# Kernel optimization log

Measured on AMD Instinct MI355X. Metric: run time of the kernel, lower is better.

## Reference

```python
import jax, jax.numpy as jnp
import numpy as np

E = 1024
H = 16
F = 4096
B, S = 4, 2048
LN_EPS = 1e-5


def setup_inputs() -> dict:
    key = jax.random.key(0)
    ks = jax.random.split(key, 12)
    sE = 1.0 / np.sqrt(E)
    sF = 1.0 / np.sqrt(F)
    return {
        "x": jax.random.normal(ks[0], (B, S, E), dtype=jnp.float32),
        # attention projections (torch Linear weight layout [out,in], bias=False)
        "Wq": jax.random.uniform(ks[1], (E, E), jnp.float32, -sE, sE),
        "Wk": jax.random.uniform(ks[2], (E, E), jnp.float32, -sE, sE),
        "Wv": jax.random.uniform(ks[3], (E, E), jnp.float32, -sE, sE),
        "Wo": jax.random.uniform(ks[4], (E, E), jnp.float32, -sE, sE),
        # LayerNorms
        "g1": jnp.ones((E,), jnp.float32),
        "b1": jnp.zeros((E,), jnp.float32),
        "g2": jnp.ones((E,), jnp.float32),
        "b2": jnp.zeros((E,), jnp.float32),
        # FFN (classical): linear1 [F,E], linear2 [E,F]
        "W1": jax.random.uniform(ks[5], (F, E), jnp.float32, -sE, sE),
        "bb1": jax.random.uniform(ks[6], (F,), jnp.float32, -sE, sE),
        "W2": jax.random.uniform(ks[7], (E, F), jnp.float32, -sF, sF),
        "bb2": jax.random.uniform(ks[8], (F,), jnp.float32, -sF, sF)[:E] * 0 + jax.random.uniform(ks[9], (E,), jnp.float32, -sF, sF),
    }


def _layernorm(x, g, b):
    mu = jnp.mean(x, axis=-1, keepdims=True)
    var = jnp.mean(jnp.square(x - mu), axis=-1, keepdims=True)
    return (x - mu) * jax.lax.rsqrt(var + LN_EPS) * g + b


def reference(x, Wq, Wk, Wv, Wo, g1, b1, g2, b2, W1, bb1, W2, bb2):
    b, s, _ = x.shape
    hd = E // H
    # projections: torch Linear is x @ W.T
    q = (x @ Wq.T).reshape(b, s, H, hd).transpose(0, 2, 1, 3)  # [B,H,S,hd]
    k = (x @ Wk.T).reshape(b, s, H, hd).transpose(0, 2, 1, 3)
    v = (x @ Wv.T).reshape(b, s, H, hd).transpose(0, 2, 1, 3)
    scores = jnp.einsum('bhqd,bhkd->bhqk', q, k) / jnp.sqrt(jnp.float32(hd))
    probs = jax.nn.softmax(scores, axis=-1)
    attn = jnp.einsum('bhqk,bhkd->bhqd', probs, v)
    attn = attn.transpose(0, 2, 1, 3).reshape(b, s, E)
    attn_out = attn @ Wo.T
    # residual + LN (dropout=0 / eval)
    h = _layernorm(x + attn_out, g1, b1)
    # FFN
    ffn = jax.nn.relu(h @ W1.T + bb1) @ W2.T + bb2
    return _layernorm(h + ffn, g2, b2)
```

## Files before the change

### kernel.cpp

```cpp
#include <hip/hip_runtime.h>
#include <stdint.h>

#define E_DIM   1024
#define H_NUM   16
#define HD      64
#define F_DIM   4096
#define B_NUM   4
#define S_LEN   2048
#define M_ROWS  (B_NUM * S_LEN)
#define QKV_LD  3072

typedef unsigned short u16;
typedef __bf16 bf16_t;
typedef bf16_t  bf16x8 __attribute__((ext_vector_type(8)));
typedef u16     u16x8  __attribute__((ext_vector_type(8)));
typedef float   f32x4  __attribute__((ext_vector_type(4)));
typedef float   f32x16 __attribute__((ext_vector_type(16)));
typedef unsigned u32x4 __attribute__((ext_vector_type(4)));

#define AS1 __attribute__((address_space(1)))
#define AS3 __attribute__((address_space(3)))

__device__ __forceinline__ void gload_lds16(const void* g, void* l) {
    __builtin_amdgcn_global_load_lds((AS1 void*)g, (AS3 void*)l, 16, 0, 0);
}

__device__ __forceinline__ u16 f2b(float f) {
    union { float f; unsigned u; } a; a.f = f;
    unsigned u = a.u + 0x7fffu + ((a.u >> 16) & 1u);
    return (u16)(u >> 16);
}
__device__ __forceinline__ float b2f(u16 v) {
    union { unsigned u; float f; } a; a.u = ((unsigned)v) << 16;
    return a.f;
}

__device__ __forceinline__ unsigned cvt_pk_bf16(float lo, float hi) {
    unsigned r;
    asm("v_cvt_pk_bf16_f32 %0, %1, %2" : "=v"(r) : "v"(lo), "v"(hi));
    return r;
}

__device__ __forceinline__ int swz_c(int row) {
    return ((row & 7) << 4) ^ ((row & 8) << 2);
}
__device__ __forceinline__ int swz8(int row) {
    return (row & 7) << 4;
}

#define VM_WAIT(n) asm volatile("s_waitcnt vmcnt(" #n ")" ::: "memory")

struct CastArgs {
    const float* src[7];
    u16* dst[7];
    unsigned cum4[8];
};

__global__ __launch_bounds__(256) void cast_multi(CastArgs a) {
    const int total = a.cum4[7];
    const int stride = gridDim.x * blockDim.x;
    for (int i = blockIdx.x * blockDim.x + threadIdx.x; i < total; i += stride) {
        int s = 0;
#pragma unroll
        for (int k = 1; k < 7; ++k) s += (i >= (int)a.cum4[k]);
        const int off = i - (int)a.cum4[s];
        float4 v = reinterpret_cast<const float4*>(a.src[s])[off];
        ushort4 o;
        o.x = f2b(v.x); o.y = f2b(v.y); o.z = f2b(v.z); o.w = f2b(v.w);
        reinterpret_cast<ushort4*>(a.dst[s])[off] = o;
    }
}

__device__ __forceinline__ void store_c(float* C, size_t idx, float v) { C[idx] = v; }
__device__ __forceinline__ void store_c(u16* C, size_t idx, float v)   { C[idx] = f2b(v); }

template <typename OutT, bool RELU, bool HASBIAS, int K>
__global__ __launch_bounds__(512, 4)
void gemm2(const u16* __restrict__ A, const u16* __restrict__ B,
           OutT* __restrict__ C, const float* __restrict__ bias,
           int M, int N) {
    constexpr int NT = K / 32;
    __shared__ __align__(16) char smem[3 * 24576];

    const int tid  = threadIdx.x;
    const int lane = tid & 63, wave = tid >> 6;
    const int lr   = lane & 15, kh = lane >> 4;
    const int wr   = wave >> 2, wc = wave & 3;

    const int nwg = gridDim.x * gridDim.y;
    int wg = blockIdx.y * gridDim.x + blockIdx.x;
    const int cpx = nwg >> 3;
    wg = (wg & 7) * cpx + (wg >> 3);
    const int bx = wg % gridDim.x, by = wg / gridDim.x;
    const int row0 = by * 128, col0 = bx * 256;

    const int srow = tid >> 2, scolb = (tid & 3) * 16;
    const char* Ag  = (const char*)(A + (size_t)(row0 + srow) * K) + scolb;
    const char* Bg0 = (const char*)(B + (size_t)(col0 + srow) * K) + scolb;
    const char* Bg1 = (const char*)(B + (size_t)(col0 + 128 + srow) * K) + scolb;
    const int ldsw = wave * 1024;

    auto stage = [&](int t) {
        char* s = smem + (t % 3) * 24576;
        const size_t ko = (size_t)t * 64;
        gload_lds16(Ag + ko,  s + ldsw);
        gload_lds16(Bg0 + ko, s + 8192 + ldsw);
        gload_lds16(Bg1 + ko, s + 16384 + ldsw);
    };

    f32x4 acc[4][4] = {};
    stage(0); stage(1);

    for (int t = 0; t < NT; ++t) {
        if (t + 1 < NT) VM_WAIT(3);
        else            VM_WAIT(0);
        __builtin_amdgcn_s_barrier();
        __builtin_amdgcn_sched_barrier(0);
        if (t + 2 < NT) stage(t + 2);

        const char* s = smem + (t % 3) * 24576;
        bf16x8 af[4], bf[4];
#pragma unroll
        for (int m = 0; m < 4; ++m)
            af[m] = *(const bf16x8*)(s + (wr * 64 + m * 16 + lr) * 64 + kh * 16);
#pragma unroll
        for (int n = 0; n < 4; ++n)
            bf[n] = *(const bf16x8*)(s + 8192 + (wc * 64 + n * 16 + lr) * 64 + kh * 16);

        __builtin_amdgcn_s_setprio(1);
#pragma unroll
        for (int m = 0; m < 4; ++m)
#pragma unroll
            for (int n = 0; n < 4; ++n)
                acc[m][n] = __builtin_amdgcn_mfma_f32_16x16x32_bf16(af[m], bf[n], acc[m][n], 0, 0, 0);
        __builtin_amdgcn_s_setprio(0);
    }

#pragma unroll
    for (int m = 0; m < 4; ++m) {
#pragma unroll
        for (int n = 0; n < 4; ++n) {
            int col = col0 + wc * 64 + n * 16 + lr;
            float bv = 0.f;
            if constexpr (HASBIAS) bv = bias[col];
#pragma unroll
            for (int r = 0; r < 4; ++r) {
                int row = row0 + wr * 64 + m * 16 + kh * 4 + r;
                float v = acc[m][n][r] + bv;
                if constexpr (RELU) v = fmaxf(v, 0.f);
                store_c(C, (size_t)row * N + col, v);
            }
        }
    }
}

template <typename OutT, bool RELU, bool HASBIAS, int K>
__global__ __launch_bounds__(256, 3)
void gemm2h(const u16* __restrict__ A, const u16* __restrict__ B,
            OutT* __restrict__ C, const float* __restrict__ bias,
            int M, int N) {
    constexpr int NT = K / 32;
    __shared__ __align__(16) char smem[3 * 16384];

    const int tid  = threadIdx.x;
    const int lane = tid & 63, wave = tid >> 6;
    const int lr   = lane & 15, kh = lane >> 4;
    const int wr   = wave >> 1, wc = wave & 1;

    const int nwg = gridDim.x * gridDim.y;
    int wg = blockIdx.y * gridDim.x + blockIdx.x;
    const int cpx = nwg >> 3;
    wg = (wg & 7) * cpx + (wg >> 3);
    const int bx = wg % gridDim.x, by = wg / gridDim.x;
    const int row0 = by * 128, col0 = bx * 128;

    const int srow = tid >> 2;
    const int scolb = (tid & 3) * 16;
    const char* Ag = (const char*)(A + (size_t)(row0 + srow) * K) + scolb;
    const char* Bg = (const char*)(B + (size_t)(col0 + srow) * K) + scolb;
    const size_t rstep = (size_t)64 * K * 2;

    auto do_stage = [&](int t) {
        char* s = smem + (t % 3) * 16384;
        const size_t ko = (size_t)t * 64;
        gload_lds16(Ag + ko,         s + tid * 16);
        gload_lds16(Ag + rstep + ko, s + 4096 + tid * 16);
        gload_lds16(Bg + ko,         s + 8192 + tid * 16);
        gload_lds16(Bg + rstep + ko, s + 12288 + tid * 16);
    };

    f32x4 acc[4][4] = {};
    do_stage(0); do_stage(1);

    for (int t = 0; t < NT; ++t) {
        if (t + 1 < NT) VM_WAIT(4);
        else            VM_WAIT(0);
        __builtin_amdgcn_s_barrier();
        __builtin_amdgcn_sched_barrier(0);
        if (t + 2 < NT) do_stage(t + 2);

        const char* s = smem + (t % 3) * 16384;
        bf16x8 af[4], bf[4];
#pragma unroll
        for (int m = 0; m < 4; ++m)
            af[m] = *(const bf16x8*)(s + (wr * 64 + m * 16 + lr) * 64 + kh * 16);
#pragma unroll
        for (int n = 0; n < 4; ++n)
            bf[n] = *(const bf16x8*)(s + 8192 + (wc * 64 + n * 16 + lr) * 64 + kh * 16);

        __builtin_amdgcn_s_setprio(1);
#pragma unroll
        for (int m = 0; m < 4; ++m)
#pragma unroll
            for (int n = 0; n < 4; ++n)
                acc[m][n] = __builtin_amdgcn_mfma_f32_16x16x32_bf16(af[m], bf[n], acc[m][n], 0, 0, 0);
        __builtin_amdgcn_s_setprio(0);
    }

#pragma unroll
    for (int m = 0; m < 4; ++m) {
#pragma unroll
        for (int n = 0; n < 4; ++n) {
            int col = col0 + wc * 64 + n * 16 + lr;
            float bv = 0.f;
            if constexpr (HASBIAS) bv = bias[col];
#pragma unroll
            for (int r = 0; r < 4; ++r) {
                int row = row0 + wr * 64 + m * 16 + kh * 4 + r;
                float v = acc[m][n][r] + bv;
                if constexpr (RELU) v = fmaxf(v, 0.f);
                store_c(C, (size_t)row * N + col, v);
            }
        }
    }
}

#define SC_LOG2E 0.1803368801111204f

__global__ __launch_bounds__(256, 4)
void attn_kernel(const u16* __restrict__ QKV, u16* __restrict__ Ob) {
    __shared__ char Ks[2][64 * 128];
    __shared__ char Vt[2][64 * 128];

    const int tid  = threadIdx.x;
    const int lane = tid & 63, wave = tid >> 6;
    const int l31  = lane & 31, hi = lane >> 5;
    const int q0   = blockIdx.x * 128;
    const int h    = blockIdx.y;
    const int b    = blockIdx.z;

    const u16* Q  = QKV;
    const u16* Kp = QKV + 1024;
    const u16* V  = QKV + 2048;

    const size_t qrow = (size_t)(b * S_LEN + q0 + wave * 32 + l31);
    bf16x8 qf[4];
#pragma unroll
    for (int c = 0; c < 4; ++c) {
        qf[c] = *(const bf16x8*)(Q + qrow * QKV_LD + h * HD + c * 16 + hi * 8);
#pragma unroll
        for (int j = 0; j < 8; ++j)
            qf[c][j] = (bf16_t)((float)qf[c][j] * SC_LOG2E);
    }

    f32x16 o0 = {}, o1 = {};
    float l_run = 0.f;

    const u16* Vg = V + (size_t)(b * S_LEN) * QKV_LD + h * HD;
    const char* Kg = (const char*)(Kp + (size_t)(b * S_LEN) * QKV_LD + h * HD);

    int kst_row[2], kst_colb[2], kst_lds[2];
#pragma unroll
    for (int j = 0; j < 2; ++j) {
        const int ob = (wave * 2 + j) * 1024 + lane * 16;
        kst_row[j]  = ob >> 7;
        kst_colb[j] = (ob & 127) ^ swz_c(kst_row[j]);
        kst_lds[j]  = (wave * 2 + j) * 1024;
    }
    const int vkv = wave * 16;
    const int krd = l31 * 128;
    const int vrd = l31 * 128;

    u16 vst[16];
#pragma unroll
    for (int j = 0; j < 2; ++j)
        gload_lds16(Kg + (size_t)kst_row[j] * (QKV_LD * 2) + kst_colb[j], Ks[0] + kst_lds[j]);
    {
        const u16* vp = Vg + (size_t)vkv * QKV_LD + lane;
#pragma unroll
        for (int i = 0; i < 16; ++i) vst[i] = vp[(size_t)i * QKV_LD];
        u16x8 va, vb;
#pragma unroll
        for (int i = 0; i < 4; ++i) {
            va[i] = vst[i];     va[4 + i] = vst[8 + i];
            vb[i] = vst[4 + i]; vb[4 + i] = vst[12 + i];
        }
        *(u16x8*)(Vt[0] + lane * 128 + ((vkv * 2) ^ swz8(lane)))      = va;
        *(u16x8*)(Vt[0] + lane * 128 + ((vkv * 2 + 16) ^ swz8(lane))) = vb;
    }
    __syncthreads();

    const int NT = S_LEN / 64;
    for (int t = 0; t < NT; ++t) {
        const int cur = t & 1;
        if (t < NT - 1) {
            const int kv0n = (t + 1) * 64;
#pragma unroll
            for (int j = 0; j < 2; ++j)
                gload_lds16(Kg + (size_t)(kv0n + kst_row[j]) * (QKV_LD * 2) + kst_colb[j],
                            Ks[cur ^ 1] + kst_lds[j]);
            const u16* vp = Vg + (size_t)(kv0n + vkv) * QKV_LD + lane;
#pragma unroll
            for (int i = 0; i < 16; ++i) vst[i] = vp[(size_t)i * QKV_LD];
        }

#pragma unroll
        for (int half = 0; half < 2; ++half) {
            const char* ksb = Ks[cur] + half * 4096 + krd;
            f32x16 st = {};
#pragma unroll
            for (int c = 0; c < 4; ++c) {
                bf16x8 kf = *(const bf16x8*)(ksb + ((c * 32 + hi * 16) ^ swz_c(l31)));
                st = __builtin_amdgcn_mfma_f32_32x32x16_bf16(kf, qf[c], st, 0, 0, 0);
            }

            float rs0 = 0.f, rs1 = 0.f, rs2 = 0.f, rs3 = 0.f;
#pragma unroll
            for (int i = 0; i < 16; i += 4) {
                st[i]     = exp2f(st[i]);
                st[i + 1] = exp2f(st[i + 1]);
                st[i + 2] = exp2f(st[i + 2]);
                st[i + 3] = exp2f(st[i + 3]);
                rs0 += st[i]; rs1 += st[i + 1]; rs2 += st[i + 2]; rs3 += st[i + 3];
            }
            float rs = (rs0 + rs1) + (rs2 + rs3);
            rs += __shfl_xor(rs, 32);
            l_run += rs;

            unsigned w[8];
#pragma unroll
            for (int i = 0; i < 8; ++i) w[i] = cvt_pk_bf16(st[2 * i], st[2 * i + 1]);

#pragma unroll
            for (int cc = 0; cc < 2; ++cc) {
                u32x4 fw;
                fw[0] = w[4 * cc];     fw[1] = w[4 * cc + 1];
                fw[2] = w[4 * cc + 2]; fw[3] = w[4 * cc + 3];
                bf16x8 pf = __builtin_bit_cast(bf16x8, fw);
                const int colb = (half * 64 + cc * 32 + hi * 16) ^ swz8(l31);
                bf16x8 v0 = *(const bf16x8*)(Vt[cur] + vrd + colb);
                bf16x8 v1 = *(const bf16x8*)(Vt[cur] + 4096 + vrd + colb);
                o0 = __builtin_amdgcn_mfma_f32_32x32x16_bf16(v0, pf, o0, 0, 0, 0);
                o1 = __builtin_amdgcn_mfma_f32_32x32x16_bf16(v1, pf, o1, 0, 0, 0);
            }
        }

        if (t < NT - 1) {
            u16x8 va, vb;
#pragma unroll
            for (int i = 0; i < 4; ++i) {
                va[i] = vst[i];     va[4 + i] = vst[8 + i];
                vb[i] = vst[4 + i]; vb[4 + i] = vst[12 + i];
            }
            *(u16x8*)(Vt[cur ^ 1] + lane * 128 + ((vkv * 2) ^ swz8(lane)))      = va;
            *(u16x8*)(Vt[cur ^ 1] + lane * 128 + ((vkv * 2 + 16) ^ swz8(lane))) = vb;
        }
        __syncthreads();
    }

    const float inv = 1.0f / l_run;
    unsigned m0[16], xx[16];
#pragma unroll
    for (int g = 0; g < 4; ++g)
#pragma unroll
        for (int u = 0; u < 2; ++u) {
            int r = g * 4 + 2 * u;
            m0[2 * g + u]     = cvt_pk_bf16(o0[r] * inv, o0[r + 1] * inv);
            m0[8 + 2 * g + u] = cvt_pk_bf16(o1[r] * inv, o1[r + 1] * inv);
        }
#pragma unroll
    for (int i = 0; i < 16; ++i) xx[i] = __shfl_xor(m0[i], 32);

    {
        unsigned full[8], sec[8];
#pragma unroll
        for (int g = 0; g < 4; ++g) {
            full[2 * g + 0] = hi ? xx[8 + 2 * g]     : m0[2 * g];
            full[2 * g + 1] = hi ? xx[8 + 2 * g + 1] : m0[2 * g + 1];
            sec[2 * g + 0]  = hi ? m0[8 + 2 * g]     : xx[2 * g];
            sec[2 * g + 1]  = hi ? m0[8 + 2 * g + 1] : xx[2 * g + 1];
        }
        u32x4 out0, out1, out2, out3;
        out0[0] = full[0]; out0[1] = full[1]; out0[2] = sec[0]; out0[3] = sec[1];
        out1[0] = full[2]; out1[1] = full[3]; out1[2] = sec[2]; out1[3] = sec[3];
        out2[0] = full[4]; out2[1] = full[5]; out2[2] = sec[4]; out2[3] = sec[5];
        out3[0] = full[6]; out3[1] = full[7]; out3[2] = sec[6]; out3[3] = sec[7];
        u16* op = Ob + qrow * E_DIM + h * HD + hi * 32;
        *(u32x4*)(op)      = out0;
        *(u32x4*)(op + 8)  = out1;
        *(u32x4*)(op + 16) = out2;
        *(u32x4*)(op + 24) = out3;
    }
}

template <typename XA, typename XB>
__device__ __forceinline__ float4 ld4(const XA* p, size_t idx) {
    if constexpr (sizeof(XA) == 2) {
        ushort4 v = reinterpret_cast<const ushort4*>(p)[idx];
        float4 o; o.x = b2f(v.x); o.y = b2f(v.y); o.z = b2f(v.z); o.w = b2f(v.w);
        return o;
    } else {
        return reinterpret_cast<const float4*>(p)[idx];
    }
}

template <typename XA, typename XB>
__global__ __launch_bounds__(256)
void add_ln(const XA* __restrict__ xa, const XB* __restrict__ xb2,
            const float* __restrict__ g, const float* __restrict__ be,
            float* __restrict__ of, u16* __restrict__ ob) {
    const int row = blockIdx.x;
    const int t = threadIdx.x;
    const int lane = t & 63, wave = t >> 6;

    float4 va = ld4<XA, XB>(xa + (size_t)row * E_DIM, t);
    float4 vb = ld4<XB, XA>(xb2 + (size_t)row * E_DIM, t);
    float v0 = va.x + vb.x, v1 = va.y + vb.y, v2 = va.z + vb.z, v3 = va.w + vb.w;
    float s  = v0 + v1 + v2 + v3;
    float s2 = v0 * v0 + v1 * v1 + v2 * v2 + v3 * v3;
#pragma unroll
    for (int m = 32; m >= 1; m >>= 1) {
        s  += __shfl_xor(s, m);
        s2 += __shfl_xor(s2, m);
    }
    __shared__ float red[8];
    if (lane == 0) { red[wave] = s; red[4 + wave] = s2; }
    __syncthreads();
    s  = red[0] + red[1] + red[2] + red[3];
    s2 = red[4] + red[5] + red[6] + red[7];

    float mu   = s * (1.0f / E_DIM);
    float var  = s2 * (1.0f / E_DIM) - mu * mu;
    float rstd = rsqrtf(var + 1e-5f);

    float4 gg = reinterpret_cast<const float4*>(g)[t];
    float4 bb = reinterpret_cast<const float4*>(be)[t];
    float y0 = (v0 - mu) * rstd * gg.x + bb.x;
    float y1 = (v1 - mu) * rstd * gg.y + bb.y;
    float y2 = (v2 - mu) * rstd * gg.z + bb.z;
    float y3 = (v3 - mu) * rstd * gg.w + bb.w;
    if (of) {
        float4 o; o.x = y0; o.y = y1; o.z = y2; o.w = y3;
        reinterpret_cast<float4*>(of + (size_t)row * E_DIM)[t] = o;
    }
    if (ob) {
        ushort4 o;
        o.x = f2b(y0); o.y = f2b(y1); o.z = f2b(y2); o.w = f2b(y3);
        reinterpret_cast<ushort4*>(ob + (size_t)row * E_DIM)[t] = o;
    }
}

extern "C" void kernel_launch(void* const* d_in, const int* in_sizes, int n_in,
                              void* d_out, int out_size, void* d_ws, size_t ws_size,
                              hipStream_t stream) {
    const float* x   = (const float*)d_in[0];
    const float* Wq  = (const float*)d_in[1];
    const float* Wk  = (const float*)d_in[2];
    const float* Wv  = (const float*)d_in[3];
    const float* Wo  = (const float*)d_in[4];
    const float* g1  = (const float*)d_in[5];
    const float* b1  = (const float*)d_in[6];
    const float* g2  = (const float*)d_in[7];
    const float* b2  = (const float*)d_in[8];
    const float* W1  = (const float*)d_in[9];
    const float* bb1 = (const float*)d_in[10];
    const float* W2  = (const float*)d_in[11];
    const float* bb2 = (const float*)d_in[12];
    float* out = (float*)d_out;

    char* ws = (char*)d_ws;
    const size_t MB = 1024ull * 1024ull;
    u16* wqkvb = (u16*)(ws + 0 * MB);
    u16* wob   = (u16*)(ws + 6 * MB);
    u16* w1b   = (u16*)(ws + 8 * MB);
    u16* w2b   = (u16*)(ws + 16 * MB);
    u16* xb    = (u16*)(ws + 24 * MB);
    u16* qkvb  = (u16*)(ws + 40 * MB);
    u16* attnb = (u16*)(ws + 88 * MB);
    u16* attno = (u16*)(ws + 104 * MB);
    u16* hb    = (u16*)(ws + 136 * MB);
    u16* ffn1  = (u16*)(ws + 24 * MB);
    u16* y2b   = (u16*)(ws + 104 * MB);

    dim3 blk(256);

    CastArgs ca;
    ca.src[0] = x;   ca.dst[0] = xb;
    ca.src[1] = Wq;  ca.dst[1] = wqkvb;
    ca.src[2] = Wk;  ca.dst[2] = wqkvb + E_DIM * E_DIM;
    ca.src[3] = Wv;  ca.dst[3] = wqkvb + 2 * E_DIM * E_DIM;
    ca.src[4] = Wo;  ca.dst[4] = wob;
    ca.src[5] = W1;  ca.dst[5] = w1b;
    ca.src[6] = W2;  ca.dst[6] = w2b;
    unsigned n4[7] = {M_ROWS * E_DIM / 4, E_DIM * E_DIM / 4, E_DIM * E_DIM / 4,
                      E_DIM * E_DIM / 4, E_DIM * E_DIM / 4, F_DIM * E_DIM / 4,
                      E_DIM * F_DIM / 4};
    ca.cum4[0] = 0;
    for (int i = 0; i < 7; ++i) ca.cum4[i + 1] = ca.cum4[i] + n4[i];
    cast_multi<<<dim3(2048), blk, 0, stream>>>(ca);

    dim3 blk5(512);
    gemm2<u16, false, false, E_DIM><<<dim3(QKV_LD / 256, M_ROWS / 128), blk5, 0, stream>>>(
        xb, wqkvb, qkvb, nullptr, M_ROWS, QKV_LD);

    attn_kernel<<<dim3(S_LEN / 128, H_NUM, B_NUM), blk, 0, stream>>>(qkvb, attnb);

    gemm2h<u16, false, false, E_DIM><<<dim3(E_DIM / 128, M_ROWS / 128), blk, 0, stream>>>(
        attnb, wob, attno, nullptr, M_ROWS, E_DIM);

    add_ln<float, u16><<<dim3(M_ROWS), blk, 0, stream>>>(x, attno, g1, b1, nullptr, hb);

    gemm2<u16, true, true, E_DIM><<<dim3(F_DIM / 256, M_ROWS / 128), blk5, 0, stream>>>(
        hb, w1b, ffn1, bb1, M_ROWS, F_DIM);

    gemm2h<u16, false, true, F_DIM><<<dim3(E_DIM / 128, M_ROWS / 128), blk, 0, stream>>>(
        ffn1, w2b, y2b, bb2, M_ROWS, E_DIM);

    add_ln<u16, u16><<<dim3(M_ROWS), blk, 0, stream>>>(hb, y2b, g2, b2, out, nullptr);
}
```

Measured before the change: 392.4 us.

## Emit V pre-transposed and swizzled from QKV GEMM; fold softmax scale into Wq

The QKV projection GEMM now writes the V columns directly into a per-head transposed, swizzled global layout. This lets the attention kernel stream V tiles into LDS with async global_load_lds, in place of strided 2-byte gathers followed by register shuffles and LDS stores. The softmax scale times log2(e) is folded into Wq during the bf16 cast, which removes the per-element Q scaling in attention. The cost is a scattered 8-byte-store epilogue for V in the GEMM, an extra workspace buffer, and a slightly different rounding order for the Q scaling.

```diff
diff --git a/kernel.cpp b/kernel.cpp
--- a/kernel.cpp
+++ b/kernel.cpp
@@ -49,10 +49,12 @@
 }
 
 #define VM_WAIT(n) asm volatile("s_waitcnt vmcnt(" #n ")" ::: "memory")
+#define SC_LOG2E 0.1803368801111204f
 
 struct CastArgs {
     const float* src[7];
     u16* dst[7];
+    float scale[7];
     unsigned cum4[8];
 };
 
@@ -64,9 +66,10 @@
 #pragma unroll
         for (int k = 1; k < 7; ++k) s += (i >= (int)a.cum4[k]);
         const int off = i - (int)a.cum4[s];
+        const float sc = a.scale[s];
         float4 v = reinterpret_cast<const float4*>(a.src[s])[off];
         ushort4 o;
-        o.x = f2b(v.x); o.y = f2b(v.y); o.z = f2b(v.z); o.w = f2b(v.w);
+        o.x = f2b(v.x * sc); o.y = f2b(v.y * sc); o.z = f2b(v.z * sc); o.w = f2b(v.w * sc);
         reinterpret_cast<ushort4*>(a.dst[s])[off] = o;
     }
 }
@@ -74,11 +77,11 @@
 __device__ __forceinline__ void store_c(float* C, size_t idx, float v) { C[idx] = v; }
 __device__ __forceinline__ void store_c(u16* C, size_t idx, float v)   { C[idx] = f2b(v); }
 
-template <typename OutT, bool RELU, bool HASBIAS, int K>
+template <typename OutT, bool RELU, bool HASBIAS, int K, bool VSPLIT>
 __global__ __launch_bounds__(512, 4)
 void gemm2(const u16* __restrict__ A, const u16* __restrict__ B,
            OutT* __restrict__ C, const float* __restrict__ bias,
-           int M, int N) {
+           char* __restrict__ VtG, int M, int N) {
     constexpr int NT = K / 32;
     __shared__ __align__(16) char smem[3 * 24576];
 
@@ -134,6 +137,31 @@
             for (int n = 0; n < 4; ++n)
                 acc[m][n] = __builtin_amdgcn_mfma_f32_16x16x32_bf16(af[m], bf[n], acc[m][n], 0, 0, 0);
         __builtin_amdgcn_s_setprio(0);
+    }
+
+    if (VSPLIT && col0 >= 2048) {
+#pragma unroll
+        for (int m = 0; m < 4; ++m) {
+#pragma unroll
+            for (int n = 0; n < 4; ++n) {
+                const int colv = col0 - 2048 + wc * 64 + n * 16 + lr;
+                const int h = colv >> 6, d = colv & 63;
+                const int rowq = row0 + wr * 64 + m * 16 + kh * 4;
+                const int bq = rowq >> 11, sq = rowq & 2047;
+                const int kvt = sq >> 6, kl = sq & 63;
+                const int g = kl >> 4, qb = kl & 12;
+                const int slotq = ((qb & 4) << 1) | ((qb & 8) >> 1) | (qb & 3);
+                const size_t byte_off = ((size_t)((bq * H_NUM + h) * HD + d) << 12)
+                                        + kvt * 128 + ((((g << 4) + slotq) << 1) ^ swz8(d));
+                const u16 p0 = f2b(acc[m][n][0]), p1 = f2b(acc[m][n][1]);
+                const u16 p2 = f2b(acc[m][n][2]), p3 = f2b(acc[m][n][3]);
+                uint2 pk;
+                pk.x = (unsigned)p0 | ((unsigned)p1 << 16);
+                pk.y = (unsigned)p2 | ((unsigned)p3 << 16);
+                *(uint2*)(VtG + byte_off) = pk;
+            }
+        }
+        return;
     }
 
 #pragma unroll
@@ -235,10 +263,9 @@
     }
 }
 
-#define SC_LOG2E 0.1803368801111204f
-
 __global__ __launch_bounds__(256, 4)
-void attn_kernel(const u16* __restrict__ QKV, u16* __restrict__ Ob) {
+void attn_kernel(const u16* __restrict__ QKV, const char* __restrict__ VtG,
+                 u16* __restrict__ Ob) {
     __shared__ char Ks[2][64 * 128];
     __shared__ char Vt[2][64 * 128];
 
@@ -251,52 +278,35 @@
 
     const u16* Q  = QKV;
     const u16* Kp = QKV + 1024;
-    const u16* V  = QKV + 2048;
 
     const size_t qrow = (size_t)(b * S_LEN + q0 + wave * 32 + l31);
     bf16x8 qf[4];
 #pragma unroll
-    for (int c = 0; c < 4; ++c) {
+    for (int c = 0; c < 4; ++c)
         qf[c] = *(const bf16x8*)(Q + qrow * QKV_LD + h * HD + c * 16 + hi * 8);
-#pragma unroll
-        for (int j = 0; j < 8; ++j)
-            qf[c][j] = (bf16_t)((float)qf[c][j] * SC_LOG2E);
-    }
 
     f32x16 o0 = {}, o1 = {};
     float l_run = 0.f;
 
-    const u16* Vg = V + (size_t)(b * S_LEN) * QKV_LD + h * HD;
-    const char* Kg = (const char*)(Kp + (size_t)(b * S_LEN) * QKV_LD + h * HD);
-
-    int kst_row[2], kst_colb[2], kst_lds[2];
+    const char* Kg  = (const char*)(Kp + (size_t)(b * S_LEN) * QKV_LD + h * HD);
+    const char* Vgb = VtG + ((size_t)((b * H_NUM + h) * HD) << 12);
+
+    int st_row[2], st_colb[2], st_lds[2], kst_colb[2];
 #pragma unroll
     for (int j = 0; j < 2; ++j) {
         const int ob = (wave * 2 + j) * 1024 + lane * 16;
-        kst_row[j]  = ob >> 7;
-        kst_colb[j] = (ob & 127) ^ swz_c(kst_row[j]);
-        kst_lds[j]  = (wave * 2 + j) * 1024;
-    }
-    const int vkv = wave * 16;
+        st_row[j]   = ob >> 7;
+        st_colb[j]  = ob & 127;
+        kst_colb[j] = (ob & 127) ^ swz_c(st_row[j]);
+        st_lds[j]   = (wave * 2 + j) * 1024;
+    }
     const int krd = l31 * 128;
     const int vrd = l31 * 128;
 
-    u16 vst[16];
-#pragma unroll
-    for (int j = 0; j < 2; ++j)
-        gload_lds16(Kg + (size_t)kst_row[j] * (QKV_LD * 2) + kst_colb[j], Ks[0] + kst_lds[j]);
-    {
-        const u16* vp = Vg + (size_t)vkv * QKV_LD + lane;
-#pragma unroll
-        for (int i = 0; i < 16; ++i) vst[i] = vp[(size_t)i * QKV_LD];
-        u16x8 va, vb;
-#pragma unroll
-        for (int i = 0; i < 4; ++i) {
-            va[i] = vst[i];     va[4 + i] = vst[8 + i];
-            vb[i] = vst[4 + i]; vb[4 + i] = vst[12 + i];
-        }
-        *(u16x8*)(Vt[0] + lane * 128 + ((vkv * 2) ^ swz8(lane)))      = va;
-        *(u16x8*)(Vt[0] + lane * 128 + ((vkv * 2 + 16) ^ swz8(lane))) = vb;
+#pragma unroll
+    for (int j = 0; j < 2; ++j) {
+        gload_lds16(Kg + (size_t)st_row[j] * (QKV_LD * 2) + kst_colb[j], Ks[0] + st_lds[j]);
+        gload_lds16(Vgb + (size_t)st_row[j] * 4096 + st_colb[j],         Vt[0] + st_lds[j]);
     }
     __syncthreads();
 
@@ -306,12 +316,12 @@
         if (t < NT - 1) {
             const int kv0n = (t + 1) * 64;
 #pragma unroll
-            for (int j = 0; j < 2; ++j)
-                gload_lds16(Kg + (size_t)(kv0n + kst_row[j]) * (QKV_LD * 2) + kst_colb[j],
-                            Ks[cur ^ 1] + kst_lds[j]);
-            const u16* vp = Vg + (size_t)(kv0n + vkv) * QKV_LD + lane;
-#pragma unroll
-            for (int i = 0; i < 16; ++i) vst[i] = vp[(size_t)i * QKV_LD];
+            for (int j = 0; j < 2; ++j) {
+                gload_lds16(Kg + (size_t)(kv0n + st_row[j]) * (QKV_LD * 2) + kst_colb[j],
+                            Ks[cur ^ 1] + st_lds[j]);
+                gload_lds16(Vgb + (size_t)st_row[j] * 4096 + (t + 1) * 128 + st_colb[j],
+                            Vt[cur ^ 1] + st_lds[j]);
+            }
         }
 
 #pragma unroll
@@ -353,17 +363,6 @@
                 o0 = __builtin_amdgcn_mfma_f32_32x32x16_bf16(v0, pf, o0, 0, 0, 0);
                 o1 = __builtin_amdgcn_mfma_f32_32x32x16_bf16(v1, pf, o1, 0, 0, 0);
             }
-        }
-
-        if (t < NT - 1) {
-            u16x8 va, vb;
-#pragma unroll
-            for (int i = 0; i < 4; ++i) {
-                va[i] = vst[i];     va[4 + i] = vst[8 + i];
-                vb[i] = vst[4 + i]; vb[4 + i] = vst[12 + i];
-            }
-            *(u16x8*)(Vt[cur ^ 1] + lane * 128 + ((vkv * 2) ^ swz8(lane)))      = va;
-            *(u16x8*)(Vt[cur ^ 1] + lane * 128 + ((vkv * 2 + 16) ^ swz8(lane))) = vb;
         }
         __syncthreads();
     }
@@ -489,19 +488,20 @@
     u16* attnb = (u16*)(ws + 88 * MB);
     u16* attno = (u16*)(ws + 104 * MB);
     u16* hb    = (u16*)(ws + 136 * MB);
+    char* VtG  = (ws + 152 * MB);
     u16* ffn1  = (u16*)(ws + 24 * MB);
     u16* y2b   = (u16*)(ws + 104 * MB);
 
     dim3 blk(256);
 
     CastArgs ca;
-    ca.src[0] = x;   ca.dst[0] = xb;
-    ca.src[1] = Wq;  ca.dst[1] = wqkvb;
-    ca.src[2] = Wk;  ca.dst[2] = wqkvb + E_DIM * E_DIM;
-    ca.src[3] = Wv;  ca.dst[3] = wqkvb + 2 * E_DIM * E_DIM;
-    ca.src[4] = Wo;  ca.dst[4] = wob;
-    ca.src[5] = W1;  ca.dst[5] = w1b;
-    ca.src[6] = W2;  ca.dst[6] = w2b;
+    ca.src[0] = x;   ca.dst[0] = xb;                            ca.scale[0] = 1.f;
+    ca.src[1] = Wq;  ca.dst[1] = wqkvb;                         ca.scale[1] = SC_LOG2E;
+    ca.src[2] = Wk;  ca.dst[2] = wqkvb + E_DIM * E_DIM;         ca.scale[2] = 1.f;
+    ca.src[3] = Wv;  ca.dst[3] = wqkvb + 2 * E_DIM * E_DIM;     ca.scale[3] = 1.f;
+    ca.src[4] = Wo;  ca.dst[4] = wob;                           ca.scale[4] = 1.f;
+    ca.src[5] = W1;  ca.dst[5] = w1b;                           ca.scale[5] = 1.f;
+    ca.src[6] = W2;  ca.dst[6] = w2b;                           ca.scale[6] = 1.f;
     unsigned n4[7] = {M_ROWS * E_DIM / 4, E_DIM * E_DIM / 4, E_DIM * E_DIM / 4,
                       E_DIM * E_DIM / 4, E_DIM * E_DIM / 4, F_DIM * E_DIM / 4,
                       E_DIM * F_DIM / 4};
@@ -510,18 +510,18 @@
     cast_multi<<<dim3(2048), blk, 0, stream>>>(ca);
 
     dim3 blk5(512);
-    gemm2<u16, false, false, E_DIM><<<dim3(QKV_LD / 256, M_ROWS / 128), blk5, 0, stream>>>(
-        xb, wqkvb, qkvb, nullptr, M_ROWS, QKV_LD);
-
-    attn_kernel<<<dim3(S_LEN / 128, H_NUM, B_NUM), blk, 0, stream>>>(qkvb, attnb);
+    gemm2<u16, false, false, E_DIM, true><<<dim3(QKV_LD / 256, M_ROWS / 128), blk5, 0, stream>>>(
+        xb, wqkvb, qkvb, nullptr, VtG, M_ROWS, QKV_LD);
+
+    attn_kernel<<<dim3(S_LEN / 128, H_NUM, B_NUM), blk, 0, stream>>>(qkvb, VtG, attnb);
 
     gemm2h<u16, false, false, E_DIM><<<dim3(E_DIM / 128, M_ROWS / 128), blk, 0, stream>>>(
         attnb, wob, attno, nullptr, M_ROWS, E_DIM);
 
     add_ln<float, u16><<<dim3(M_ROWS), blk, 0, stream>>>(x, attno, g1, b1, nullptr, hb);
 
-    gemm2<u16, true, true, E_DIM><<<dim3(F_DIM / 256, M_ROWS / 128), blk5, 0, stream>>>(
-        hb, w1b, ffn1, bb1, M_ROWS, F_DIM);
+    gemm2<u16, true, true, E_DIM, false><<<dim3(F_DIM / 256, M_ROWS / 128), blk5, 0, stream>>>(
+        hb, w1b, ffn1, bb1, nullptr, M_ROWS, F_DIM);
 
     gemm2h<u16, false, true, F_DIM><<<dim3(E_DIM / 128, M_ROWS / 128), blk, 0, stream>>>(
         ffn1, w2b, y2b, bb2, M_ROWS, E_DIM);
```

Result: faster. 383.6 us (-2.2%).
